# Kernel tuning notes

Hardware: AMD Instinct MI355X
Metric: run time of the kernel (lower is better)

Reference implementation:

```python
import jax, jax.numpy as jnp
import numpy as np

JACCARD_THRESH = 0.5
NEGPOS_RATIO = 3
V0, V1 = 0.1, 0.2  # SSD encoding variances


def setup_inputs() -> dict:
    key = jax.random.key(0)
    k1, k2, k3, k4, k5, k6, k7 = jax.random.split(key, 7)
    B, P, C, O = 128, 8732, 21, 16
    loc_data = jax.random.normal(k1, (B, P, 4), dtype=jnp.float32)
    conf_data = jax.random.normal(k2, (B, P, C), dtype=jnp.float32)
    # default boxes in center form (cx, cy, w, h), all in [0,1]
    cxcy = jax.random.uniform(k3, (P, 2), minval=0.05, maxval=0.95)
    wh = jax.random.uniform(k4, (P, 2), minval=0.05, maxval=0.6)
    dbox_list = jnp.concatenate([cxcy, wh], axis=1).astype(jnp.float32)
    # ground-truth boxes in corner form with guaranteed positive extent
    tl = jax.random.uniform(k5, (B, O, 2), minval=0.0, maxval=0.6)
    sz = jax.random.uniform(k6, (B, O, 2), minval=0.05, maxval=0.35)
    labels = jax.random.randint(k7, (B, O, 1), 0, C - 1).astype(jnp.float32)
    targets = jnp.concatenate([tl, tl + sz, labels], axis=2)
    return {"loc_data": loc_data, "conf_data": conf_data,
            "dbox_list": dbox_list, "targets": targets}


def _match_one(truths, labels, dbox):
    """SSD match for one image. truths:[O,4] corner, labels:[O], dbox:[P,4] center."""
    pf = jnp.concatenate([dbox[:, :2] - dbox[:, 2:] * 0.5,
                          dbox[:, :2] + dbox[:, 2:] * 0.5], axis=1)  # point form [P,4]
    lt = jnp.maximum(truths[:, None, :2], pf[None, :, :2])
    rb = jnp.minimum(truths[:, None, 2:], pf[None, :, 2:])
    whi = jnp.clip(rb - lt, 0.0)
    inter = whi[..., 0] * whi[..., 1]                                # [O,P]
    area_t = (truths[:, 2] - truths[:, 0]) * (truths[:, 3] - truths[:, 1])
    area_p = dbox[:, 2] * dbox[:, 3]
    ov = inter / (area_t[:, None] + area_p[None, :] - inter)         # jaccard [O,P]
    best_prior_idx = jnp.argmax(ov, axis=1)                          # [O]
    bto = jnp.max(ov, axis=0)                                        # [P]
    bti = jnp.argmax(ov, axis=0)                                     # [P]
    bto = bto.at[best_prior_idx].set(2.0)
    O = truths.shape[0]
    bti = jax.lax.fori_loop(0, O, lambda j, b: b.at[best_prior_idx[j]].set(j), bti)
    matched = truths[bti]                                            # [P,4]
    conf = labels[bti].astype(jnp.int32) + 1
    conf = jnp.where(bto < JACCARD_THRESH, 0, conf)
    g_cxcy = ((matched[:, :2] + matched[:, 2:]) * 0.5 - dbox[:, :2]) / (V0 * dbox[:, 2:])
    g_wh = jnp.log((matched[:, 2:] - matched[:, :2]) / dbox[:, 2:]) / V1
    return jnp.concatenate([g_cxcy, g_wh], axis=1), conf


def reference(loc_data, conf_data, dbox_list, targets):
    B, P, C = conf_data.shape
    loc_t, conf_t = jax.vmap(_match_one, in_axes=(0, 0, None))(
        targets[..., :4], targets[..., 4], dbox_list)
    pos = conf_t > 0                                                  # [B,P]
    # smooth L1 (beta=1), summed over positives
    ad = jnp.abs(loc_data - loc_t)
    sl1 = jnp.where(ad < 1.0, 0.5 * ad * ad, ad - 0.5)
    loss_l = jnp.sum(jnp.where(pos[..., None], sl1, 0.0))
    # per-prior cross entropy
    logp = jax.nn.log_softmax(conf_data, axis=-1)
    ce = -jnp.take_along_axis(logp, conf_t[..., None], axis=-1)[..., 0]  # [B,P]
    # hard negative mining via double argsort (rank in descending order)
    ce_neg = jnp.where(pos, 0.0, ce)
    loss_idx = jnp.argsort(-ce_neg, axis=1)
    idx_rank = jnp.argsort(loss_idx, axis=1)
    num_pos = jnp.sum(pos, axis=1, keepdims=True)
    num_neg = jnp.minimum(num_pos * NEGPOS_RATIO, P)
    neg = idx_rank < num_neg
    sel = pos | neg
    loss_c = jnp.sum(jnp.where(sel, ce, 0.0))
    N = jnp.sum(num_pos).astype(loc_data.dtype)
    return jnp.stack([loss_l / N, loss_c / N])
```

## Files before the change

### kernel.cpp

```cpp
#include <hip/hip_runtime.h>
#include <cstddef>

#define Bn 128
#define Pn 8732
#define Cn 21
#define On 16
#define MAGIC 0x13579BDFu

__device__ __forceinline__ void argmax_combine(float& v, int& p, float v2, int p2) {
  if (v2 > v || (v2 == v && p2 < p)) { v = v2; p = p2; }
}

__global__ __launch_bounds__(256) void stream_kernel(
    const float* __restrict__ conf, const float* __restrict__ dbox,
    const float* __restrict__ targets,
    float* __restrict__ ce0, unsigned char* __restrict__ pack,
    unsigned long long* __restrict__ keys) {
  const int wb = threadIdx.x >> 6, lane = threadIdx.x & 63;
  const int wave_g = blockIdx.x * 4 + wb;
  const int b = wave_g & 127;
  const int cg = wave_g >> 7;

  __shared__ float4 s_row4[4][336];
  __shared__ float s_tt[4][On * 5];
  __shared__ float s_ar[4][On];

  if (lane < On * 5) s_tt[wb][lane] = targets[(size_t)b * On * 5 + lane];
  if (lane < On) {
    float x1 = targets[(size_t)b * On * 5 + lane * 5 + 0];
    float y1 = targets[(size_t)b * On * 5 + lane * 5 + 1];
    float x2 = targets[(size_t)b * On * 5 + lane * 5 + 2];
    float y2 = targets[(size_t)b * On * 5 + lane * 5 + 3];
    s_ar[wb][lane] = (x2 - x1) * (y2 - y1);
  }

  float bestv[On]; int bestp[On];
  #pragma unroll
  for (int j = 0; j < On; j++) { bestv[j] = -1.0f; bestp[j] = 0x7fffffff; }

  #pragma unroll
  for (int i = 0; i < 5; i++) {
    const int ci = cg + 32 * i;
    if (ci >= 137) break;
    const int p0 = ci * 64;
    const int rows = min(64, Pn - p0);
    const int n4 = rows * Cn / 4;

    const float4* src = (const float4*)(conf + ((size_t)b * Pn + p0) * Cn);
    float4 v0, v1, v2, v3, v4, v5;
    if (lane < n4)        v0 = src[lane];
    if (lane + 64 < n4)   v1 = src[lane + 64];
    if (lane + 128 < n4)  v2 = src[lane + 128];
    if (lane + 192 < n4)  v3 = src[lane + 192];
    if (lane + 256 < n4)  v4 = src[lane + 256];
    if (lane + 320 < n4)  v5 = src[lane + 320];
    if (lane < n4)        s_row4[wb][lane] = v0;
    if (lane + 64 < n4)   s_row4[wb][lane + 64] = v1;
    if (lane + 128 < n4)  s_row4[wb][lane + 128] = v2;
    if (lane + 192 < n4)  s_row4[wb][lane + 192] = v3;
    if (lane + 256 < n4)  s_row4[wb][lane + 256] = v4;
    if (lane + 320 < n4)  s_row4[wb][lane + 320] = v5;

    if (lane < rows) {
      const int p = p0 + lane;
      const float* x = (const float*)s_row4[wb] + lane * Cn;
      float m = x[0];
      #pragma unroll
      for (int q = 1; q < Cn; q++) m = fmaxf(m, x[q]);
      float s = 0.0f;
      #pragma unroll
      for (int q = 0; q < Cn; q++) s += expf(x[q] - m);
      float lse = m + logf(s);
      ce0[(size_t)b * Pn + p] = lse - x[0];

      float4 d = ((const float4*)dbox)[p];
      float px1 = d.x - d.z * 0.5f, py1 = d.y - d.w * 0.5f;
      float px2 = d.x + d.z * 0.5f, py2 = d.y + d.w * 0.5f;
      float ap = d.z * d.w;
      float mv = -1.0f; int mj = 0;
      #pragma unroll
      for (int j = 0; j < On; j++) {
        float lx = fmaxf(s_tt[wb][j*5+0], px1);
        float ly = fmaxf(s_tt[wb][j*5+1], py1);
        float rx = fminf(s_tt[wb][j*5+2], px2);
        float ry = fminf(s_tt[wb][j*5+3], py2);
        float w = fmaxf(rx - lx, 0.0f), h = fmaxf(ry - ly, 0.0f);
        float inter = w * h;
        float ov = inter / (s_ar[wb][j] + ap - inter);
        if (ov > bestv[j]) { bestv[j] = ov; bestp[j] = p; }
        if (ov > mv) { mv = ov; mj = j; }
      }
      pack[(size_t)b * Pn + p] =
          (unsigned char)(mj | ((mv >= 0.5f) ? 16 : 0));
    }
  }

  #pragma unroll
  for (int j = 0; j < On; j++) {
    float v = bestv[j]; int p = bestp[j];
    #pragma unroll
    for (int off = 32; off; off >>= 1) {
      float v2 = __shfl_down(v, off);
      int p2 = __shfl_down(p, off);
      argmax_combine(v, p, v2, p2);
    }
    if (lane == 0) {
      unsigned long long key;
      if (v < 0.0f) key = 0xC000000000000000ull;
      else key = (((unsigned long long)(__float_as_uint(v) | 0xC0000000u)) << 32)
               | (unsigned long long)(0xFFFFFFFFu - (unsigned)p);
      atomicMax(&keys[b * On + j], key);
    }
  }
}

__global__ __launch_bounds__(1024) void reduce_kernel(
    const float* __restrict__ loc, const float* __restrict__ conf,
    const float* __restrict__ dbox, const float* __restrict__ targets,
    const float* __restrict__ ce0, const unsigned char* __restrict__ pack,
    const unsigned long long* __restrict__ keys,
    unsigned int* __restrict__ res, float* __restrict__ out) {
  const int b = blockIdx.x;
  const int tid = threadIdx.x;
  const int wave = tid >> 6, lane = tid & 63;

  __shared__ float s_t[On * 5];
  __shared__ int s_bp[On];
  __shared__ unsigned hist[16][256];
  __shared__ float s_redf[2][16];
  __shared__ int s_redi[16];
  __shared__ unsigned s_prefix;
  __shared__ int s_kk;
  __shared__ int s_np;

  if (tid < On * 5) s_t[tid] = targets[(size_t)b * On * 5 + tid];
  if (tid < On)
    s_bp[tid] = (int)(0xFFFFFFFFu - (unsigned)(keys[b * On + tid] & 0xFFFFFFFFull));
  __syncthreads();

  float ce_r[9];
  float my_loc = 0.0f, my_cep = 0.0f; int my_np = 0;
  #pragma unroll
  for (int sI = 0; sI < 9; sI++) {
    ce_r[sI] = 0.0f;
    const int p = tid + 1024 * sI;
    if (p < Pn) {
      unsigned char pk = pack[(size_t)b * Pn + p];
      float c0 = ce0[(size_t)b * Pn + p];
      int pos = pk >> 4;
      int bt = pk & 15;
      #pragma unroll
      for (int j = 0; j < On; j++)
        if (s_bp[j] == p) { bt = j; pos = 1; }
      ce_r[sI] = pos ? 0.0f : c0;
      if (pos) {
        my_np++;
        const float* t = &s_t[bt * 5];
        int c = (int)t[4] + 1;
        const float* row = conf + ((size_t)b * Pn + p) * Cn;
        my_cep += c0 + row[0] - row[c];
        float4 d = ((const float4*)dbox)[p];
        float mx1 = t[0], my1 = t[1], mx2 = t[2], my2 = t[3];
        float g0 = ((mx1 + mx2) * 0.5f - d.x) / (0.1f * d.z);
        float g1 = ((my1 + my2) * 0.5f - d.y) / (0.1f * d.w);
        float g2 = logf((mx2 - mx1) / d.z) / 0.2f;
        float g3 = logf((my2 - my1) / d.w) / 0.2f;
        float4 ld = ((const float4*)loc)[(size_t)b * Pn + p];
        float g[4] = {g0, g1, g2, g3};
        float l[4] = {ld.x, ld.y, ld.z, ld.w};
        #pragma unroll
        for (int q = 0; q < 4; q++) {
          float ad = fabsf(l[q] - g[q]);
          my_loc += (ad < 1.0f) ? 0.5f * ad * ad : ad - 0.5f;
        }
      }
    }
  }

  {
    int np = my_np;
    #pragma unroll
    for (int off = 32; off; off >>= 1) np += __shfl_down(np, off);
    if (lane == 0) s_redi[wave] = np;
  }
  __syncthreads();
  if (tid == 0) {
    int np = 0;
    #pragma unroll
    for (int w = 0; w < 16; w++) np += s_redi[w];
    s_np = np;
  }
  __syncthreads();

  const int k = min(s_np * 3, Pn);
  unsigned prefix = 0, maskb = 0;
  int kk = k;
  for (int shift = 24; shift >= 0; shift -= 8) {
    #pragma unroll
    for (int j = 0; j < 4; j++) hist[wave][lane * 4 + j] = 0;
    __syncthreads();
    #pragma unroll
    for (int sI = 0; sI < 9; sI++) {
      const int p = tid + 1024 * sI;
      if (p < Pn) {
        unsigned u = __float_as_uint(ce_r[sI]);
        if ((u & maskb) == prefix) atomicAdd(&hist[wave][(u >> shift) & 255u], 1u);
      }
    }
    __syncthreads();
    if (tid < 256) {
      unsigned c = 0;
      #pragma unroll
      for (int w = 0; w < 16; w++) c += hist[w][tid];
      hist[0][tid] = c;
    }
    __syncthreads();
    if (tid == 0) {
      int cum = 0, chosen = 0;
      for (int bin = 255; bin >= 0; bin--) {
        int c = (int)hist[0][bin];
        if (cum + c >= kk) { chosen = bin; break; }
        cum += c;
      }
      s_prefix = prefix | ((unsigned)chosen << shift);
      s_kk = kk - cum;
    }
    __syncthreads();
    prefix = s_prefix; kk = s_kk;
    maskb |= 255u << shift;
    __syncthreads();
  }
  float T = __uint_as_float(prefix);

  float sum_gt = 0.0f; int cnt_gt = 0;
  #pragma unroll
  for (int sI = 0; sI < 9; sI++) {
    const int p = tid + 1024 * sI;
    if (p < Pn) {
      float x = ce_r[sI];
      if (x > T) { sum_gt += x; cnt_gt++; }
    }
  }
  #pragma unroll
  for (int off = 32; off; off >>= 1) {
    sum_gt += __shfl_down(sum_gt, off);
    cnt_gt += __shfl_down(cnt_gt, off);
    my_loc += __shfl_down(my_loc, off);
    my_cep += __shfl_down(my_cep, off);
  }
  if (lane == 0) {
    s_redf[0][wave] = my_loc; s_redf[1][wave] = sum_gt + my_cep; s_redi[wave] = cnt_gt;
  }
  __syncthreads();
  if (tid == 0) {
    float ll = 0.0f, lc = 0.0f; int cg = 0;
    #pragma unroll
    for (int w = 0; w < 16; w++) {
      ll += s_redf[0][w]; lc += s_redf[1][w]; cg += s_redi[w];
    }
    lc += (k > 0) ? (float)(k - cg) * T : 0.0f;
    atomicExch(&res[b * 4 + 0], __float_as_uint(ll));
    atomicExch(&res[b * 4 + 1], __float_as_uint(lc));
    atomicExch(&res[b * 4 + 2], (unsigned)s_np);
    __threadfence();
    atomicExch(&res[b * 4 + 3], MAGIC);
  }

  if (b == 0 && tid < 64) {
    float ll = 0.0f, lc = 0.0f; int np = 0;
    #pragma unroll
    for (int h = 0; h < 2; h++) {
      const int i = tid + 64 * h;
      while (atomicAdd(&res[i * 4 + 3], 0u) != MAGIC) { __builtin_amdgcn_s_sleep(8); }
      ll += __uint_as_float(atomicAdd(&res[i * 4 + 0], 0u));
      lc += __uint_as_float(atomicAdd(&res[i * 4 + 1], 0u));
      np += (int)atomicAdd(&res[i * 4 + 2], 0u);
    }
    #pragma unroll
    for (int off = 32; off; off >>= 1) {
      ll += __shfl_down(ll, off);
      lc += __shfl_down(lc, off);
      np += __shfl_down(np, off);
    }
    if (tid == 0) {
      float fN = (float)np;
      out[0] = ll / fN;
      out[1] = lc / fN;
    }
  }
}

extern "C" void kernel_launch(void* const* d_in, const int* in_sizes, int n_in,
                              void* d_out, int out_size, void* d_ws, size_t ws_size,
                              hipStream_t stream) {
  const float* loc_data  = (const float*)d_in[0];
  const float* conf_data = (const float*)d_in[1];
  const float* dbox      = (const float*)d_in[2];
  const float* targets   = (const float*)d_in[3];
  float* out = (float*)d_out;

  char* ws = (char*)d_ws;
  float* ce0 = (float*)ws;
  unsigned char* pack = (unsigned char*)(ws + (size_t)Bn * Pn * 4);
  unsigned long long* keys =
      (unsigned long long*)(ws + (size_t)Bn * Pn * 5);
  unsigned int* res = (unsigned int*)(ws + (size_t)Bn * Pn * 5 + Bn * On * 8);

  stream_kernel<<<1024, 256, 0, stream>>>(conf_data, dbox, targets, ce0, pack, keys);
  reduce_kernel<<<Bn, 1024, 0, stream>>>(loc_data, conf_data, dbox, targets,
                                         ce0, pack, keys, res, out);
}
```

Baseline: 233.1 us.

## Fuse matching/CE streaming and reduction into one per-image kernel using LDS

Merges the streaming kernel and the per-image reduce kernel into a single kernel with one 1024-thread block per image. Per-prior CE and match info stay in LDS instead of a global workspace, and the per-truth best prior is reduced in LDS rather than with global 64-bit atomicMax. Conf chunk loads are double-buffered in registers to overlap with the softmax and IoU math. The serial 256-bin scan in the radix select is replaced with a parallel suffix scan. The trade-off is that the bandwidth-heavy streaming phase now runs on only 128 blocks with large LDS use, which may leave many CUs idle.

```diff
diff --git a/kernel.cpp b/kernel.cpp
--- a/kernel.cpp
+++ b/kernel.cpp
@@ -11,59 +11,69 @@
   if (v2 > v || (v2 == v && p2 < p)) { v = v2; p = p2; }
 }
 
-__global__ __launch_bounds__(256) void stream_kernel(
-    const float* __restrict__ conf, const float* __restrict__ dbox,
-    const float* __restrict__ targets,
-    float* __restrict__ ce0, unsigned char* __restrict__ pack,
-    unsigned long long* __restrict__ keys) {
-  const int wb = threadIdx.x >> 6, lane = threadIdx.x & 63;
-  const int wave_g = blockIdx.x * 4 + wb;
-  const int b = wave_g & 127;
-  const int cg = wave_g >> 7;
-
-  __shared__ float4 s_row4[4][336];
-  __shared__ float s_tt[4][On * 5];
-  __shared__ float s_ar[4][On];
-
-  if (lane < On * 5) s_tt[wb][lane] = targets[(size_t)b * On * 5 + lane];
-  if (lane < On) {
-    float x1 = targets[(size_t)b * On * 5 + lane * 5 + 0];
-    float y1 = targets[(size_t)b * On * 5 + lane * 5 + 1];
-    float x2 = targets[(size_t)b * On * 5 + lane * 5 + 2];
-    float y2 = targets[(size_t)b * On * 5 + lane * 5 + 3];
-    s_ar[wb][lane] = (x2 - x1) * (y2 - y1);
-  }
+__global__ __launch_bounds__(1024) void fused_kernel(
+    const float* __restrict__ loc, const float* __restrict__ conf,
+    const float* __restrict__ dbox, const float* __restrict__ targets,
+    unsigned int* __restrict__ res, float* __restrict__ out) {
+  const int b = blockIdx.x;
+  const int tid = threadIdx.x;
+  const int wv = tid >> 6, lane = tid & 63;
+
+  __shared__ float s_ce[Pn];
+  __shared__ float s_stage[16][1344];
+  __shared__ unsigned char s_bti[Pn];
+  __shared__ unsigned hist[16][256];
+  __shared__ float s_tt[80];
+  __shared__ float s_ar[On];
+  __shared__ float s_mv[On][16];
+  __shared__ int   s_mp[On][16];
+  __shared__ int   s_bp[On];
+  __shared__ float s_redf[2][16];
+  __shared__ int   s_redi[16];
+  __shared__ int   s_sfx[256];
+  __shared__ int   s_wsum[4];
+  __shared__ unsigned s_prefix;
+  __shared__ int s_kk, s_np;
+
+  if (tid < 80) s_tt[tid] = targets[b * 80 + tid];
+  __syncthreads();
+  if (tid < On)
+    s_ar[tid] = (s_tt[tid*5+2] - s_tt[tid*5+0]) * (s_tt[tid*5+3] - s_tt[tid*5+1]);
+  __syncthreads();
 
   float bestv[On]; int bestp[On];
   #pragma unroll
   for (int j = 0; j < On; j++) { bestv[j] = -1.0f; bestp[j] = 0x7fffffff; }
 
-  #pragma unroll
-  for (int i = 0; i < 5; i++) {
-    const int ci = cg + 32 * i;
-    if (ci >= 137) break;
-    const int p0 = ci * 64;
-    const int rows = min(64, Pn - p0);
-    const int n4 = rows * Cn / 4;
-
-    const float4* src = (const float4*)(conf + ((size_t)b * Pn + p0) * Cn);
-    float4 v0, v1, v2, v3, v4, v5;
-    if (lane < n4)        v0 = src[lane];
-    if (lane + 64 < n4)   v1 = src[lane + 64];
-    if (lane + 128 < n4)  v2 = src[lane + 128];
-    if (lane + 192 < n4)  v3 = src[lane + 192];
-    if (lane + 256 < n4)  v4 = src[lane + 256];
-    if (lane + 320 < n4)  v5 = src[lane + 320];
-    if (lane < n4)        s_row4[wb][lane] = v0;
-    if (lane + 64 < n4)   s_row4[wb][lane + 64] = v1;
-    if (lane + 128 < n4)  s_row4[wb][lane + 128] = v2;
-    if (lane + 192 < n4)  s_row4[wb][lane + 192] = v3;
-    if (lane + 256 < n4)  s_row4[wb][lane + 256] = v4;
-    if (lane + 320 < n4)  s_row4[wb][lane + 320] = v5;
+  const size_t confBase = (size_t)b * Pn * Cn;
+  const int nch = (136 - wv) / 16 + 1;
+  float4 rg[2][6];
+
+  auto load_chunk = [&](float4 (&r)[6], int ci) {
+    const int n4 = (ci == 136) ? 147 : 336;
+    const float4* src = (const float4*)(conf + confBase + (size_t)ci * 64 * Cn);
+    #pragma unroll
+    for (int q = 0; q < 6; q++)
+      if (lane + 64*q < n4) r[q] = src[lane + 64*q];
+  };
+
+  load_chunk(rg[0], wv);
+  for (int i = 0; i < nch; i++) {
+    const int ci = wv + 16 * i;
+    const int n4 = (ci == 136) ? 147 : 336;
+    const int rows = (ci == 136) ? 28 : 64;
+    float4 (&cur)[6] = rg[i & 1];
+    {
+      float4* dst = (float4*)s_stage[wv];
+      #pragma unroll
+      for (int q = 0; q < 6; q++)
+        if (lane + 64*q < n4) dst[lane + 64*q] = cur[q];
+    }
+    if (i + 1 < nch) load_chunk(rg[(i + 1) & 1], ci + 16);
 
     if (lane < rows) {
-      const int p = p0 + lane;
-      const float* x = (const float*)s_row4[wb] + lane * Cn;
+      const int p = ci * 64 + lane;
+      const float* x = s_stage[wv] + lane * Cn;
       float m = x[0];
       #pragma unroll
       for (int q = 1; q < Cn; q++) m = fmaxf(m, x[q]);
@@ -71,7 +81,7 @@
       #pragma unroll
       for (int q = 0; q < Cn; q++) s += expf(x[q] - m);
       float lse = m + logf(s);
-      ce0[(size_t)b * Pn + p] = lse - x[0];
+      s_ce[p] = lse - x[0];
 
       float4 d = ((const float4*)dbox)[p];
       float px1 = d.x - d.z * 0.5f, py1 = d.y - d.w * 0.5f;
@@ -80,18 +90,17 @@
       float mv = -1.0f; int mj = 0;
       #pragma unroll
       for (int j = 0; j < On; j++) {
-        float lx = fmaxf(s_tt[wb][j*5+0], px1);
-        float ly = fmaxf(s_tt[wb][j*5+1], py1);
-        float rx = fminf(s_tt[wb][j*5+2], px2);
-        float ry = fminf(s_tt[wb][j*5+3], py2);
+        float lx = fmaxf(s_tt[j*5+0], px1);
+        float ly = fmaxf(s_tt[j*5+1], py1);
+        float rx = fminf(s_tt[j*5+2], px2);
+        float ry = fminf(s_tt[j*5+3], py2);
         float w = fmaxf(rx - lx, 0.0f), h = fmaxf(ry - ly, 0.0f);
         float inter = w * h;
-        float ov = inter / (s_ar[wb][j] + ap - inter);
+        float ov = inter / (s_ar[j] + ap - inter);
         if (ov > bestv[j]) { bestv[j] = ov; bestp[j] = p; }
         if (ov > mv) { mv = ov; mj = j; }
       }
-      pack[(size_t)b * Pn + p] =
-          (unsigned char)(mj | ((mv >= 0.5f) ? 16 : 0));
+      s_bti[p] = (unsigned char)(mj | ((mv >= 0.5f) ? 16 : 0));
     }
   }
 
@@ -104,60 +113,39 @@
       int p2 = __shfl_down(p, off);
       argmax_combine(v, p, v2, p2);
     }
-    if (lane == 0) {
-      unsigned long long key;
-      if (v < 0.0f) key = 0xC000000000000000ull;
-      else key = (((unsigned long long)(__float_as_uint(v) | 0xC0000000u)) << 32)
-               | (unsigned long long)(0xFFFFFFFFu - (unsigned)p);
-      atomicMax(&keys[b * On + j], key);
-    }
-  }
-}
-
-__global__ __launch_bounds__(1024) void reduce_kernel(
-    const float* __restrict__ loc, const float* __restrict__ conf,
-    const float* __restrict__ dbox, const float* __restrict__ targets,
-    const float* __restrict__ ce0, const unsigned char* __restrict__ pack,
-    const unsigned long long* __restrict__ keys,
-    unsigned int* __restrict__ res, float* __restrict__ out) {
-  const int b = blockIdx.x;
-  const int tid = threadIdx.x;
-  const int wave = tid >> 6, lane = tid & 63;
-
-  __shared__ float s_t[On * 5];
-  __shared__ int s_bp[On];
-  __shared__ unsigned hist[16][256];
-  __shared__ float s_redf[2][16];
-  __shared__ int s_redi[16];
-  __shared__ unsigned s_prefix;
-  __shared__ int s_kk;
-  __shared__ int s_np;
-
-  if (tid < On * 5) s_t[tid] = targets[(size_t)b * On * 5 + tid];
-  if (tid < On)
-    s_bp[tid] = (int)(0xFFFFFFFFu - (unsigned)(keys[b * On + tid] & 0xFFFFFFFFull));
+    if (lane == 0) { s_mv[j][wv] = v; s_mp[j][wv] = p; }
+  }
+  __syncthreads();
+  if (tid < On) {
+    float v = s_mv[tid][0]; int p = s_mp[tid][0];
+    #pragma unroll
+    for (int w = 1; w < 16; w++) argmax_combine(v, p, s_mv[tid][w], s_mp[tid][w]);
+    s_bp[tid] = p;
+  }
+  __syncthreads();
+  if (tid == 0) {
+    #pragma unroll
+    for (int j = 0; j < On; j++)
+      s_bti[s_bp[j]] = (unsigned char)(j | 16);
+  }
   __syncthreads();
 
   float ce_r[9];
   float my_loc = 0.0f, my_cep = 0.0f; int my_np = 0;
   #pragma unroll
-  for (int sI = 0; sI < 9; sI++) {
-    ce_r[sI] = 0.0f;
-    const int p = tid + 1024 * sI;
+  for (int s9 = 0; s9 < 9; s9++) {
+    ce_r[s9] = 0.0f;
+    const int p = tid + 1024 * s9;
     if (p < Pn) {
-      unsigned char pk = pack[(size_t)b * Pn + p];
-      float c0 = ce0[(size_t)b * Pn + p];
-      int pos = pk >> 4;
-      int bt = pk & 15;
-      #pragma unroll
-      for (int j = 0; j < On; j++)
-        if (s_bp[j] == p) { bt = j; pos = 1; }
-      ce_r[sI] = pos ? 0.0f : c0;
+      int pk = s_bti[p];
+      float c0 = s_ce[p];
+      int pos = pk >> 4, bt = pk & 15;
+      ce_r[s9] = pos ? 0.0f : c0;
       if (pos) {
         my_np++;
-        const float* t = &s_t[bt * 5];
+        const float* t = &s_tt[bt * 5];
         int c = (int)t[4] + 1;
-        const float* row = conf + ((size_t)b * Pn + p) * Cn;
+        const float* row = conf + confBase + (size_t)p * Cn;
         my_cep += c0 + row[0] - row[c];
         float4 d = ((const float4*)dbox)[p];
         float mx1 = t[0], my1 = t[1], mx2 = t[2], my2 = t[3];
@@ -176,12 +164,11 @@
       }
     }
   }
-
   {
     int np = my_np;
     #pragma unroll
     for (int off = 32; off; off >>= 1) np += __shfl_down(np, off);
-    if (lane == 0) s_redi[wave] = np;
+    if (lane == 0) s_redi[wv] = np;
   }
   __syncthreads();
   if (tid == 0) {
@@ -193,51 +180,63 @@
   __syncthreads();
 
   const int k = min(s_np * 3, Pn);
+  int kk = max(k, 1);
   unsigned prefix = 0, maskb = 0;
-  int kk = k;
   for (int shift = 24; shift >= 0; shift -= 8) {
     #pragma unroll
-    for (int j = 0; j < 4; j++) hist[wave][lane * 4 + j] = 0;
-    __syncthreads();
-    #pragma unroll
-    for (int sI = 0; sI < 9; sI++) {
-      const int p = tid + 1024 * sI;
+    for (int j = 0; j < 4; j++) hist[wv][lane * 4 + j] = 0;
+    __syncthreads();
+    #pragma unroll
+    for (int s9 = 0; s9 < 9; s9++) {
+      const int p = tid + 1024 * s9;
       if (p < Pn) {
-        unsigned u = __float_as_uint(ce_r[sI]);
-        if ((u & maskb) == prefix) atomicAdd(&hist[wave][(u >> shift) & 255u], 1u);
-      }
-    }
-    __syncthreads();
+        unsigned u = __float_as_uint(ce_r[s9]);
+        if ((u & maskb) == prefix) atomicAdd(&hist[wv][(u >> shift) & 255u], 1u);
+      }
+    }
+    __syncthreads();
+    int v = 0;
     if (tid < 256) {
-      unsigned c = 0;
-      #pragma unroll
-      for (int w = 0; w < 16; w++) c += hist[w][tid];
-      hist[0][tid] = c;
-    }
-    __syncthreads();
-    if (tid == 0) {
-      int cum = 0, chosen = 0;
-      for (int bin = 255; bin >= 0; bin--) {
-        int c = (int)hist[0][bin];
-        if (cum + c >= kk) { chosen = bin; break; }
-        cum += c;
-      }
-      s_prefix = prefix | ((unsigned)chosen << shift);
-      s_kk = kk - cum;
+      int h = 0;
+      #pragma unroll
+      for (int w = 0; w < 16; w++) h += (int)hist[w][tid];
+      v = h;
+      #pragma unroll
+      for (int off = 1; off < 64; off <<= 1) {
+        int u2 = __shfl_down(v, off);
+        if (lane + off < 64) v += u2;
+      }
+      if (lane == 0) s_wsum[tid >> 6] = v;
+    }
+    __syncthreads();
+    if (tid < 256) {
+      int S = v;
+      #pragma unroll
+      for (int w = 0; w < 4; w++) if (w > (tid >> 6)) S += s_wsum[w];
+      s_sfx[tid] = S;
+    }
+    __syncthreads();
+    if (tid < 256) {
+      int S = s_sfx[tid];
+      int Snext = (tid == 255) ? 0 : s_sfx[tid + 1];
+      if (S >= kk && Snext < kk) {
+        s_prefix = prefix | ((unsigned)tid << shift);
+        s_kk = kk - Snext;
+      }
     }
     __syncthreads();
     prefix = s_prefix; kk = s_kk;
     maskb |= 255u << shift;
     __syncthreads();
   }
-  float T = __uint_as_float(prefix);
+  const float T = __uint_as_float(prefix);
 
   float sum_gt = 0.0f; int cnt_gt = 0;
   #pragma unroll
-  for (int sI = 0; sI < 9; sI++) {
-    const int p = tid + 1024 * sI;
+  for (int s9 = 0; s9 < 9; s9++) {
+    const int p = tid + 1024 * s9;
     if (p < Pn) {
-      float x = ce_r[sI];
+      float x = ce_r[s9];
       if (x > T) { sum_gt += x; cnt_gt++; }
     }
   }
@@ -249,7 +248,9 @@
     my_cep += __shfl_down(my_cep, off);
   }
   if (lane == 0) {
-    s_redf[0][wave] = my_loc; s_redf[1][wave] = sum_gt + my_cep; s_redi[wave] = cnt_gt;
+    s_redf[0][wv] = my_loc;
+    s_redf[1][wv] = sum_gt + my_cep;
+    s_redi[wv] = cnt_gt;
   }
   __syncthreads();
   if (tid == 0) {
@@ -258,7 +259,7 @@
     for (int w = 0; w < 16; w++) {
       ll += s_redf[0][w]; lc += s_redf[1][w]; cg += s_redi[w];
     }
-    lc += (k > 0) ? (float)(k - cg) * T : 0.0f;
+    if (k > 0) lc += (float)(k - cg) * T;
     atomicExch(&res[b * 4 + 0], __float_as_uint(ll));
     atomicExch(&res[b * 4 + 1], __float_as_uint(lc));
     atomicExch(&res[b * 4 + 2], (unsigned)s_np);
@@ -298,15 +299,7 @@
   const float* dbox      = (const float*)d_in[2];
   const float* targets   = (const float*)d_in[3];
   float* out = (float*)d_out;
-
-  char* ws = (char*)d_ws;
-  float* ce0 = (float*)ws;
-  unsigned char* pack = (unsigned char*)(ws + (size_t)Bn * Pn * 4);
-  unsigned long long* keys =
-      (unsigned long long*)(ws + (size_t)Bn * Pn * 5);
-  unsigned int* res = (unsigned int*)(ws + (size_t)Bn * Pn * 5 + Bn * On * 8);
-
-  stream_kernel<<<1024, 256, 0, stream>>>(conf_data, dbox, targets, ce0, pack, keys);
-  reduce_kernel<<<Bn, 1024, 0, stream>>>(loc_data, conf_data, dbox, targets,
-                                         ce0, pack, keys, res, out);
+  unsigned int* res = (unsigned int*)d_ws;
+
+  fused_kernel<<<Bn, 1024, 0, stream>>>(loc_data, conf_data, dbox, targets, res, out);
 }
```

After: 308.4 us. 1.32x slower.
